# Performance work log

Measured on AMD Instinct MI355X. Metric: run time of the kernel, lower is better.

Reference implementation:

```python
import jax, jax.numpy as jnp
import numpy as np

NL, NK = 10000, 2000          # ligand / keypoint node counts
ELL, EKL = 320000, 160000     # lig->lig and kp->lig edge counts
IN, HID, OUT = 128, 128, 128  # in_size, hidden_size, out_size
FDIM = 2 * IN + 1             # edge MLP input: [h_src, h_dst, dij]


def silu(x):
    return x * jax.nn.sigmoid(x)


def setup_inputs() -> dict:
    keys = iter(jax.random.split(jax.random.key(0), 64))

    def nrm(shape, scale=0.02):
        return jax.random.normal(next(keys), shape, dtype=jnp.float32) * scale

    d = {}
    d["h_lig"] = jax.random.normal(next(keys), (NL, IN), dtype=jnp.float32)
    d["h_kp"] = jax.random.normal(next(keys), (NK, IN), dtype=jnp.float32)
    d["x_lig"] = jax.random.normal(next(keys), (NL, 3), dtype=jnp.float32)
    d["x_kp"] = jax.random.normal(next(keys), (NK, 3), dtype=jnp.float32)
    # per-node normalizer (e.g. neighbor count); keep >= 1 to avoid blowup
    d["z_lig"] = jax.random.uniform(next(keys), (NL, 1), dtype=jnp.float32, minval=1.0, maxval=32.0)
    for e in ("ll", "kl"):
        d[e + "_eW1"] = nrm((FDIM, HID)); d[e + "_eb1"] = jnp.zeros((HID,), jnp.float32)
        d[e + "_eW2"] = nrm((HID, HID)); d[e + "_eb2"] = jnp.zeros((HID,), jnp.float32)
        d[e + "_aW"] = nrm((HID, 1)); d[e + "_ab"] = jnp.zeros((1,), jnp.float32)
        d[e + "_cW1"] = nrm((FDIM, HID)); d[e + "_cb1"] = jnp.zeros((HID,), jnp.float32)
        d[e + "_cW2"] = nrm((HID, HID)); d[e + "_cb2"] = jnp.zeros((HID,), jnp.float32)
        d[e + "_cW3"] = nrm((HID, 1), scale=0.001)  # xavier gain=0.001 final coord layer
    d["n_W1"] = nrm((IN + HID, HID)); d["n_b1"] = jnp.zeros((HID,), jnp.float32)
    d["n_W2"] = nrm((HID, OUT)); d["n_b2"] = jnp.zeros((OUT,), jnp.float32)
    d["ll_src"] = jax.random.randint(next(keys), (ELL,), 0, NL, dtype=jnp.int32)
    d["ll_dst"] = jax.random.randint(next(keys), (ELL,), 0, NL, dtype=jnp.int32)
    d["kl_src"] = jax.random.randint(next(keys), (EKL,), 0, NK, dtype=jnp.int32)
    d["kl_dst"] = jax.random.randint(next(keys), (EKL,), 0, NL, dtype=jnp.int32)
    return d


def _edge_messages(hs, hd, xs, xd, eW1, eb1, eW2, eb2, aW, ab, cW1, cb1, cW2, cb2, cW3):
    x_diff = xs - xd                                     # fn.u_sub_v
    dij = jnp.linalg.norm(x_diff, axis=1, keepdims=True)  # [E,1]
    x_diff = x_diff / (dij + 1.0)
    f = jnp.concatenate([hs, hd, dij], axis=1)           # [E, 2*IN+1]
    m = silu(f @ eW1 + eb1)
    m = silu(m @ eW2 + eb2)
    msg_h = m * jax.nn.sigmoid(m @ aW + ab)              # soft attention gate
    c = silu(f @ cW1 + cb1)
    c = silu(c @ cW2 + cb2)
    msg_x = (c @ cW3) * x_diff                           # use_tanh=False path
    return msg_h, msg_x


def reference(h_lig, h_kp, x_lig, x_kp, z_lig,
              ll_eW1, ll_eb1, ll_eW2, ll_eb2, ll_aW, ll_ab,
              ll_cW1, ll_cb1, ll_cW2, ll_cb2, ll_cW3,
              kl_eW1, kl_eb1, kl_eW2, kl_eb2, kl_aW, kl_ab,
              kl_cW1, kl_cb1, kl_cW2, kl_cb2, kl_cW3,
              n_W1, n_b1, n_W2, n_b2,
              ll_src, ll_dst, kl_src, kl_dst):
    # lig -> lig edges
    mh_ll, mx_ll = _edge_messages(h_lig[ll_src], h_lig[ll_dst], x_lig[ll_src], x_lig[ll_dst],
                                  ll_eW1, ll_eb1, ll_eW2, ll_eb2, ll_aW, ll_ab,
                                  ll_cW1, ll_cb1, ll_cW2, ll_cb2, ll_cW3)
    # kp -> lig edges
    mh_kl, mx_kl = _edge_messages(h_kp[kl_src], h_lig[kl_dst], x_kp[kl_src], x_lig[kl_dst],
                                  kl_eW1, kl_eb1, kl_eW2, kl_eb2, kl_aW, kl_ab,
                                  kl_cW1, kl_cb1, kl_cW2, kl_cb2, kl_cW3)
    nl = h_lig.shape[0]
    # multi_update_all with cross_reducer='sum', then per-node normalization by z
    h_neigh = (jax.ops.segment_sum(mh_ll, ll_dst, num_segments=nl)
               + jax.ops.segment_sum(mh_kl, kl_dst, num_segments=nl)) / z_lig
    x_neigh = (jax.ops.segment_sum(mx_ll, ll_dst, num_segments=nl)
               + jax.ops.segment_sum(mx_kl, kl_dst, num_segments=nl)) / z_lig
    nin = jnp.concatenate([h_lig, h_neigh], axis=1)
    h_out = h_lig + (silu(nin @ n_W1 + n_b1) @ n_W2 + n_b2)  # norm=False -> Identity
    x_out = x_lig + x_neigh
    return (h_out, x_out)
```

## Files before the change

kernel.cpp:

```cpp
#include <hip/hip_runtime.h>
#include <hip/hip_bf16.h>
#include <math.h>

#define EPB  32
#define MSTR 136
#define FSTR 264

typedef __attribute__((ext_vector_type(8))) short short8;
typedef __attribute__((ext_vector_type(4))) float f32x4;

__device__ __forceinline__ unsigned short f2bf(float x) {
    unsigned int u = __float_as_uint(x);
    u += 0x7fffu + ((u >> 16) & 1u);
    return (unsigned short)(u >> 16);
}
__device__ __forceinline__ float bf2f(short v) {
    return __uint_as_float(((unsigned int)(unsigned short)v) << 16);
}
__device__ __forceinline__ unsigned int pkbf(float a, float b) {
    __hip_bfloat162 h = __float22bfloat162_rn(make_float2(a, b));
    union { __hip_bfloat162 h2; unsigned int u; } cv; cv.h2 = h; return cv.u;
}
__device__ __forceinline__ float frcp(float x) { return __builtin_amdgcn_rcpf(x); }
__device__ __forceinline__ float fsilu(float x) {
    return x * frcp(1.0f + __expf(-x));
}
__device__ __forceinline__ float fsigm(float x) {
    return frcp(1.0f + __expf(-x));
}
__device__ __forceinline__ void atomAddF(float* p, float v) {
    unsafeAtomicAdd(p, v);
}

struct PrepArgs { const float* src[10]; };

__global__ __launch_bounds__(256) void prep_hist_kernel(PrepArgs pa, short* __restrict__ wsb,
                                                        const int* __restrict__ lld,
                                                        const int* __restrict__ kld,
                                                        int* __restrict__ hist) {
    int idx = blockIdx.x * 256 + threadIdx.x;
    if (idx < 245760) {
        int pair = idx / 49152;
        int rem  = idx - pair * 49152;
        int second = (rem >= 32768) ? 1 : 0;
        int mi = pair * 2 + second;
        int within = second ? (rem - 32768) : rem;
        int n, k, K;
        if (second) { K = 128; n = within >> 7; k = within & 127; }
        else        { K = 256; n = within >> 8; k = within & 255; }
        int dstoff = pair * 49152 + second * 32768;
        wsb[dstoff + n * K + k] = (short)f2bf(pa.src[mi][k * 128 + n]);
        return;
    }
    idx -= 245760;
    if (idx < 320000) { atomicAdd(&hist[lld[idx]], 1); return; }
    idx -= 320000;
    if (idx < 160000) atomicAdd(&hist[10000 + kld[idx]], 1);
}

__global__ __launch_bounds__(256) void scan_kernel(const int* __restrict__ hist,
                                                   int* __restrict__ cursor) {
    __shared__ int bins[10000];
    __shared__ int ps[256];
    const int b = blockIdx.x, t = threadIdx.x;
    const int* h = hist + b * 10000;
    int* cur = cursor + b * 10000;
    for (int i = t; i < 10000; i += 256) bins[i] = h[i];
    __syncthreads();
    const int base = t * 40;
    int s = 0;
#pragma unroll 8
    for (int i = 0; i < 40; i++) { int ii = base + i; if (ii < 10000) s += bins[ii]; }
    ps[t] = s;
    __syncthreads();
    for (int off = 1; off < 256; off <<= 1) {
        int v = (t >= off) ? ps[t - off] : 0;
        __syncthreads();
        ps[t] += v;
        __syncthreads();
    }
    int run = ps[t] - s;
    for (int i = 0; i < 40; i++) {
        int ii = base + i;
        if (ii < 10000) { int c = bins[ii]; bins[ii] = run; run += c; }
    }
    __syncthreads();
    for (int i = t; i < 10000; i += 256) cur[i] = bins[i];
}

struct ProjDesc { const float* A; const short* Bt; short* out; const float* bias;
                  int rows; int ktb; int co; int hasb; };
struct CArgs {
    const int *lls, *lld, *kls, *kld;
    int* cursor;
    int *ll_ssrc, *ll_sdst, *kl_ssrc, *kl_sdst;
    ProjDesc d[8];
};

__global__ __launch_bounds__(256) void scatter_proj_kernel(CArgs ca) {
    __shared__ __align__(16) short a_lds[64 * MSTR];
    const int t = threadIdx.x;
    if (blockIdx.x < 1875) {
        int i = blockIdx.x * 256 + t;
        if (i < 320000) {
            int d = ca.lld[i];
            int p = atomicAdd(&ca.cursor[d], 1);
            ca.ll_ssrc[p] = ca.lls[i]; ca.ll_sdst[p] = d;
        } else if (i < 480000) {
            int j = i - 320000;
            int d = ca.kld[j];
            int p = atomicAdd(&ca.cursor[10000 + d], 1);
            ca.kl_ssrc[p] = ca.kls[j]; ca.kl_sdst[p] = d;
        }
        return;
    }
    const int pb = blockIdx.x - 1875;
    const int di = pb / 157, tile = pb - di * 157;
    const ProjDesc pd = ca.d[di];
    if (tile * 64 >= pd.rows) return;
    {
        const int r = t >> 2, q = t & 3;
        const int node = tile * 64 + r;
        short* arow = a_lds + r * MSTR + q * 32;
        if (node < pd.rows) {
            const float* ap = pd.A + (size_t)node * 128 + q * 32;
#pragma unroll
            for (int i = 0; i < 4; i++) {
                float4 v0 = *(const float4*)(ap + i * 8);
                float4 v1 = *(const float4*)(ap + i * 8 + 4);
                uint4 o;
                o.x = pkbf(v0.x, v0.y); o.y = pkbf(v0.z, v0.w);
                o.z = pkbf(v1.x, v1.y); o.w = pkbf(v1.z, v1.w);
                *(uint4*)(arow + i * 8) = o;
            }
        } else {
            uint4 z = make_uint4(0, 0, 0, 0);
#pragma unroll
            for (int i = 0; i < 4; i++) *(uint4*)(arow + i * 8) = z;
        }
    }
    __syncthreads();

    const int ln = t & 63, wv = t >> 6;
    const int lrow = ln & 15, quad = ln >> 4;
    const int c0 = wv * 32 + lrow, c1 = c0 + 16;

    short8 bf0[4], bf1[4];
#pragma unroll
    for (int kt = 0; kt < 4; kt++) {
        bf0[kt] = *(const short8*)(pd.Bt + c0 * 256 + (pd.ktb + kt) * 32 + quad * 8);
        bf1[kt] = *(const short8*)(pd.Bt + c1 * 256 + (pd.ktb + kt) * 32 + quad * 8);
    }
    const float bb0 = pd.hasb ? pd.bias[c0] : 0.0f;
    const float bb1 = pd.hasb ? pd.bias[c1] : 0.0f;
#pragma unroll
    for (int mt = 0; mt < 4; mt++) {
        short8 af[4];
#pragma unroll
        for (int kt = 0; kt < 4; kt++)
            af[kt] = *(const short8*)(&a_lds[(mt * 16 + lrow) * MSTR + kt * 32 + quad * 8]);
        f32x4 a0 = {0.f, 0.f, 0.f, 0.f}, a1 = {0.f, 0.f, 0.f, 0.f};
#pragma unroll
        for (int kt = 0; kt < 4; kt++) {
            a0 = __builtin_amdgcn_mfma_f32_16x16x32_bf16(af[kt], bf0[kt], a0, 0, 0, 0);
            a1 = __builtin_amdgcn_mfma_f32_16x16x32_bf16(af[kt], bf1[kt], a1, 0, 0, 0);
        }
#pragma unroll
        for (int r = 0; r < 4; r++) {
            const int node = tile * 64 + mt * 16 + quad * 4 + r;
            if (node < pd.rows) {
                pd.out[(size_t)node * 256 + pd.co + c0] = (short)f2bf(a0[r] + bb0);
                pd.out[(size_t)node * 256 + pd.co + c1] = (short)f2bf(a1[r] + bb1);
            }
        }
    }
}

struct EdgeSet {
    const short *Ps, *Pd;
    const float *xs, *xd;
    const int *esrc, *edst;
    const float *w256e, *w256c;
    const short *W2t, *cW2t;
    const float *b2e, *b2c;
    const float *aW, *ab, *cW3;
};
struct EdgePair { EdgeSet s[2]; int split; };

__global__ __launch_bounds__(256, 8) void edge_kernel(EdgePair ep,
                                                      float* __restrict__ hne,
                                                      float* __restrict__ xne)
{
    __shared__ __align__(16) char mbuf[EPB * MSTR * 4];
    __shared__ float sv_l[EPB];
    __shared__ float gate_l[EPB];
    __shared__ float xdf[3][EPB];
    __shared__ int   dstl[EPB];
    __shared__ float gpc[4][EPB];
    __shared__ float gpe[4][EPB];

    short* mh = (short*)mbuf;
    short* mc = (short*)(mbuf + EPB * MSTR * 2);
    float* msg = (float*)mbuf;

    const int isKL = (blockIdx.x >= ep.split) ? 1 : 0;
    const EdgeSet P = ep.s[isKL];
    const int eb = (blockIdx.x - (isKL ? ep.split : 0)) * EPB;
    const int t = threadIdx.x;

    {
        const int e = t >> 3, q = t & 7;
        const int eid = eb + e;
        const int s = P.esrc[eid], d = P.edst[eid];
        float dx = P.xs[s * 3 + 0] - P.xd[d * 3 + 0];
        float dy = P.xs[s * 3 + 1] - P.xd[d * 3 + 1];
        float dz = P.xs[s * 3 + 2] - P.xd[d * 3 + 2];
        float dd = __builtin_amdgcn_sqrtf(dx * dx + dy * dy + dz * dz);
        if (q == 0) {
            dstl[e] = d;
            float inv = frcp(dd + 1.0f);
            xdf[0][e] = dx * inv; xdf[1][e] = dy * inv; xdf[2][e] = dz * inv;
        }
        const short* psrow = P.Ps + (size_t)s * 256 + q * 16;
        const short* pdrow = P.Pd + (size_t)d * 256 + q * 16;
#pragma unroll
        for (int path = 0; path < 2; path++) {
            const short* ps = psrow + path * 128;
            const short* pq = pdrow + path * 128;
            const float* wq = (path ? P.w256c : P.w256e) + q * 16;
            short* mrow = (path ? mc : mh) + e * MSTR + q * 16;
#pragma unroll
            for (int i = 0; i < 2; i++) {
                short8 a = *(const short8*)(ps + i * 8);
                short8 b = *(const short8*)(pq + i * 8);
                float4 wA = *(const float4*)(wq + i * 8);
                float4 wB = *(const float4*)(wq + i * 8 + 4);
                float v0 = fsilu(bf2f(a[0]) + bf2f(b[0]) + dd * wA.x);
                float v1 = fsilu(bf2f(a[1]) + bf2f(b[1]) + dd * wA.y);
                float v2 = fsilu(bf2f(a[2]) + bf2f(b[2]) + dd * wA.z);
                float v3 = fsilu(bf2f(a[3]) + bf2f(b[3]) + dd * wA.w);
                float v4 = fsilu(bf2f(a[4]) + bf2f(b[4]) + dd * wB.x);
                float v5 = fsilu(bf2f(a[5]) + bf2f(b[5]) + dd * wB.y);
                float v6 = fsilu(bf2f(a[6]) + bf2f(b[6]) + dd * wB.z);
                float v7 = fsilu(bf2f(a[7]) + bf2f(b[7]) + dd * wB.w);
                uint4 o;
                o.x = pkbf(v0, v1); o.y = pkbf(v2, v3);
                o.z = pkbf(v4, v5); o.w = pkbf(v6, v7);
                *(uint4*)(mrow + i * 8) = o;
            }
        }
    }
    __syncthreads();

    const int ln = t & 63, wv = t >> 6;
    const int lrow = ln & 15, quad = ln >> 4;
    const int c0 = wv * 32 + lrow, c1 = c0 + 16;

    {
        short8 bf0[4], bf1[4];
#pragma unroll
        for (int kt = 0; kt < 4; kt++) {
            bf0[kt] = *(const short8*)(P.cW2t + c0 * 128 + kt * 32 + quad * 8);
            bf1[kt] = *(const short8*)(P.cW2t + c1 * 128 + kt * 32 + quad * 8);
        }
        const float cw0 = P.cW3[c0], cw1 = P.cW3[c1];
        const float bb0 = P.b2c[c0], bb1 = P.b2c[c1];
#pragma unroll
        for (int mt = 0; mt < 2; mt++) {
            short8 af[4];
#pragma unroll
            for (int kt = 0; kt < 4; kt++)
                af[kt] = *(const short8*)(&mc[(mt * 16 + lrow) * MSTR + kt * 32 + quad * 8]);
            f32x4 a0 = {0.f, 0.f, 0.f, 0.f}, a1 = {0.f, 0.f, 0.f, 0.f};
#pragma unroll
            for (int kt = 0; kt < 4; kt++) {
                a0 = __builtin_amdgcn_mfma_f32_16x16x32_bf16(af[kt], bf0[kt], a0, 0, 0, 0);
                a1 = __builtin_amdgcn_mfma_f32_16x16x32_bf16(af[kt], bf1[kt], a1, 0, 0, 0);
            }
#pragma unroll
            for (int r = 0; r < 4; r++) {
                float v0 = fsilu(a0[r] + bb0);
                float v1 = fsilu(a1[r] + bb1);
                float g = v0 * cw0 + v1 * cw1;
                g += __shfl_xor(g, 1, 64);
                g += __shfl_xor(g, 2, 64);
                g += __shfl_xor(g, 4, 64);
                g += __shfl_xor(g, 8, 64);
                if (lrow == 0) gpc[wv][mt * 16 + quad * 4 + r] = g;
            }
        }
    }

    float m2s[2][8];
    {
        short8 bf0[4], bf1[4];
#pragma unroll
        for (int kt = 0; kt < 4; kt++) {
            bf0[kt] = *(const short8*)(P.W2t + c0 * 128 + kt * 32 + quad * 8);
            bf1[kt] = *(const short8*)(P.W2t + c1 * 128 + kt * 32 + quad * 8);
        }
        const float aw0 = P.aW[c0], aw1 = P.aW[c1];
        const float bb0 = P.b2e[c0], bb1 = P.b2e[c1];
#pragma unroll
        for (int mt = 0; mt < 2; mt++) {
            short8 af[4];
#pragma unroll
            for (int kt = 0; kt < 4; kt++)
                af[kt] = *(const short8*)(&mh[(mt * 16 + lrow) * MSTR + kt * 32 + quad * 8]);
            f32x4 a0 = {0.f, 0.f, 0.f, 0.f}, a1 = {0.f, 0.f, 0.f, 0.f};
#pragma unroll
            for (int kt = 0; kt < 4; kt++) {
                a0 = __builtin_amdgcn_mfma_f32_16x16x32_bf16(af[kt], bf0[kt], a0, 0, 0, 0);
                a1 = __builtin_amdgcn_mfma_f32_16x16x32_bf16(af[kt], bf1[kt], a1, 0, 0, 0);
            }
#pragma unroll
            for (int r = 0; r < 4; r++) {
                float v0 = fsilu(a0[r] + bb0);
                float v1 = fsilu(a1[r] + bb1);
                m2s[mt][r] = v0; m2s[mt][4 + r] = v1;
                float g = v0 * aw0 + v1 * aw1;
                g += __shfl_xor(g, 1, 64);
                g += __shfl_xor(g, 2, 64);
                g += __shfl_xor(g, 4, 64);
                g += __shfl_xor(g, 8, 64);
                if (lrow == 0) gpe[wv][mt * 16 + quad * 4 + r] = g;
            }
        }
    }
    __syncthreads();

    if (t < EPB) {
        sv_l[t]   = gpc[0][t] + gpc[1][t] + gpc[2][t] + gpc[3][t];
        gate_l[t] = fsigm(gpe[0][t] + gpe[1][t] + gpe[2][t] + gpe[3][t] + P.ab[0]);
    }
#pragma unroll
    for (int mt = 0; mt < 2; mt++)
#pragma unroll
        for (int r = 0; r < 4; r++) {
            const int erow = mt * 16 + quad * 4 + r;
            msg[erow * 132 + c0] = m2s[mt][r];
            msg[erow * 132 + c1] = m2s[mt][4 + r];
        }
    __syncthreads();

    if (t < 128) {
        const int col = t;
        float acc = 0.0f;
        int cur = dstl[0];
#pragma unroll 4
        for (int e = 0; e < EPB; e++) {
            const int d = dstl[e];
            if (d != cur) {
                atomAddF(&hne[(size_t)cur * 128 + col], acc);
                acc = 0.0f; cur = d;
            }
            acc += msg[e * 132 + col] * gate_l[e];
        }
        atomAddF(&hne[(size_t)cur * 128 + col], acc);
    } else if (t < 131) {
        const int ax = t - 128;
        float acc = 0.0f;
        int cur = dstl[0];
        for (int e = 0; e < EPB; e++) {
            const int d = dstl[e];
            if (d != cur) {
                atomAddF(&xne[cur * 3 + ax], acc);
                acc = 0.0f; cur = d;
            }
            acc += sv_l[e] * xdf[ax][e];
        }
        atomAddF(&xne[cur * 3 + ax], acc);
    }
}

__global__ __launch_bounds__(256) void node_kernel(
    const float* __restrict__ h_lig, const float* __restrict__ zlig,
    const short* __restrict__ W1t, const float* __restrict__ b1v,
    const short* __restrict__ W2t, const float* __restrict__ b2v,
    const float* __restrict__ x_lig,
    const float* __restrict__ acc_h, const float* __restrict__ acc_x,
    float* __restrict__ h_out, float* __restrict__ x_out)
{
    __shared__ __align__(16) short f_lds[64 * FSTR];
    __shared__ __align__(16) short m_lds[64 * MSTR];
    const int t = threadIdx.x;
    const int nb = blockIdx.x * 64;

    {
        const int e = t >> 2, q = t & 3;
        const int node = nb + e;
        short* frow = &f_lds[e * FSTR + q * 32];
        if (node < 10000) {
            const float zi = frcp(zlig[node]);
            const float4* hp = (const float4*)(h_lig + (size_t)node * 128 + q * 32);
            const float4* np = (const float4*)(acc_h + (size_t)node * 128 + q * 32);
#pragma unroll
            for (int i = 0; i < 8; i++) {
                float4 v = hp[i];
                *(uint2*)(frow + i * 4) = make_uint2(pkbf(v.x, v.y), pkbf(v.z, v.w));
            }
#pragma unroll
            for (int i = 0; i < 8; i++) {
                float4 v = np[i];
                *(uint2*)(frow + 128 + i * 4) =
                    make_uint2(pkbf(v.x * zi, v.y * zi), pkbf(v.z * zi, v.w * zi));
            }
        } else {
            const uint2 zz = make_uint2(0, 0);
#pragma unroll
            for (int i = 0; i < 8; i++) {
                *(uint2*)(frow + i * 4) = zz;
                *(uint2*)(frow + 128 + i * 4) = zz;
            }
        }
    }
    __syncthreads();

    const int ln = t & 63, wv = t >> 6;
    const int lrow = ln & 15, quad = ln >> 4;
    const int c0 = wv * 32 + lrow, c1 = c0 + 16;

    {
        short8 bf0[8], bf1[8];
#pragma unroll
        for (int kt = 0; kt < 8; kt++) {
            bf0[kt] = *(const short8*)(W1t + c0 * 256 + kt * 32 + quad * 8);
            bf1[kt] = *(const short8*)(W1t + c1 * 256 + kt * 32 + quad * 8);
        }
        const float bb0 = b1v[c0], bb1 = b1v[c1];
#pragma unroll
        for (int mt = 0; mt < 4; mt++) {
            short8 af[8];
#pragma unroll
            for (int kt = 0; kt < 8; kt++)
                af[kt] = *(const short8*)(&f_lds[(mt * 16 + lrow) * FSTR + kt * 32 + quad * 8]);
            f32x4 a0 = {0.f, 0.f, 0.f, 0.f}, a1 = {0.f, 0.f, 0.f, 0.f};
#pragma unroll
            for (int kt = 0; kt < 8; kt++) {
                a0 = __builtin_amdgcn_mfma_f32_16x16x32_bf16(af[kt], bf0[kt], a0, 0, 0, 0);
                a1 = __builtin_amdgcn_mfma_f32_16x16x32_bf16(af[kt], bf1[kt], a1, 0, 0, 0);
            }
#pragma unroll
            for (int r = 0; r < 4; r++) {
                const int erow = mt * 16 + quad * 4 + r;
                m_lds[erow * MSTR + c0] = (short)f2bf(fsilu(a0[r] + bb0));
                m_lds[erow * MSTR + c1] = (short)f2bf(fsilu(a1[r] + bb1));
            }
        }
    }
    __syncthreads();

    {
        short8 bf0[4], bf1[4];
#pragma unroll
        for (int kt = 0; kt < 4; kt++) {
            bf0[kt] = *(const short8*)(W2t + c0 * 128 + kt * 32 + quad * 8);
            bf1[kt] = *(const short8*)(W2t + c1 * 128 + kt * 32 + quad * 8);
        }
        const float bb0 = b2v[c0], bb1 = b2v[c1];
#pragma unroll
        for (int mt = 0; mt < 4; mt++) {
            short8 af[4];
#pragma unroll
            for (int kt = 0; kt < 4; kt++)
                af[kt] = *(const short8*)(&m_lds[(mt * 16 + lrow) * MSTR + kt * 32 + quad * 8]);
            f32x4 a0 = {0.f, 0.f, 0.f, 0.f}, a1 = {0.f, 0.f, 0.f, 0.f};
#pragma unroll
            for (int kt = 0; kt < 4; kt++) {
                a0 = __builtin_amdgcn_mfma_f32_16x16x32_bf16(af[kt], bf0[kt], a0, 0, 0, 0);
                a1 = __builtin_amdgcn_mfma_f32_16x16x32_bf16(af[kt], bf1[kt], a1, 0, 0, 0);
            }
#pragma unroll
            for (int r = 0; r < 4; r++) {
                const int node = nb + mt * 16 + quad * 4 + r;
                if (node < 10000) {
                    h_out[(size_t)node * 128 + c0] = a0[r] + bb0 + h_lig[(size_t)node * 128 + c0];
                    h_out[(size_t)node * 128 + c1] = a1[r] + bb1 + h_lig[(size_t)node * 128 + c1];
                }
            }
        }
    }
    if (t < 64) {
        const int node = nb + t;
        if (node < 10000) {
            const float zi = frcp(zlig[node]);
#pragma unroll
            for (int i = 0; i < 3; i++)
                x_out[node * 3 + i] = x_lig[node * 3 + i] + acc_x[node * 3 + i] * zi;
        }
    }
}

extern "C" void kernel_launch(void* const* d_in, const int* in_sizes, int n_in,
                              void* d_out, int out_size, void* d_ws, size_t ws_size,
                              hipStream_t stream)
{
    (void)in_sizes; (void)n_in; (void)ws_size; (void)out_size;
    const float* h_lig  = (const float*)d_in[0];
    const float* h_kp   = (const float*)d_in[1];
    const float* x_lig  = (const float*)d_in[2];
    const float* x_kp   = (const float*)d_in[3];
    const float* z_lig  = (const float*)d_in[4];
    const float* ll_eW1 = (const float*)d_in[5];
    const float* ll_eb1 = (const float*)d_in[6];
    const float* ll_eW2 = (const float*)d_in[7];
    const float* ll_eb2 = (const float*)d_in[8];
    const float* ll_aW  = (const float*)d_in[9];
    const float* ll_ab  = (const float*)d_in[10];
    const float* ll_cW1 = (const float*)d_in[11];
    const float* ll_cb1 = (const float*)d_in[12];
    const float* ll_cW2 = (const float*)d_in[13];
    const float* ll_cb2 = (const float*)d_in[14];
    const float* ll_cW3 = (const float*)d_in[15];
    const float* kl_eW1 = (const float*)d_in[16];
    const float* kl_eb1 = (const float*)d_in[17];
    const float* kl_eW2 = (const float*)d_in[18];
    const float* kl_eb2 = (const float*)d_in[19];
    const float* kl_aW  = (const float*)d_in[20];
    const float* kl_ab  = (const float*)d_in[21];
    const float* kl_cW1 = (const float*)d_in[22];
    const float* kl_cb1 = (const float*)d_in[23];
    const float* kl_cW2 = (const float*)d_in[24];
    const float* kl_cb2 = (const float*)d_in[25];
    const float* kl_cW3 = (const float*)d_in[26];
    const float* n_W1   = (const float*)d_in[27];
    const float* n_b1   = (const float*)d_in[28];
    const float* n_W2   = (const float*)d_in[29];
    const float* n_b2   = (const float*)d_in[30];
    const int* ll_src = (const int*)d_in[31];
    const int* ll_dst = (const int*)d_in[32];
    const int* kl_src = (const int*)d_in[33];
    const int* kl_dst = (const int*)d_in[34];

    float* h_out = (float*)d_out;
    float* x_out = h_out + 1280000;

    char* wsc = (char*)d_ws;
    short* wsb    = (short*)wsc;
    short* P_ll_s = (short*)(wsc +   491520);
    short* P_ll_d = (short*)(wsc +  5611520);
    short* P_kl_s = (short*)(wsc + 10731520);
    short* P_kl_d = (short*)(wsc + 11755520);
    int* ll_ssrc  = (int*)(wsc + 16875520);
    int* ll_sdst  = (int*)(wsc + 18155520);
    int* kl_ssrc  = (int*)(wsc + 19435520);
    int* kl_sdst  = (int*)(wsc + 20075520);
    int* hist     = (int*)(wsc + 20715520);
    int* cursor   = (int*)(wsc + 20795520);
    float* hne    = (float*)(wsc + 20875520);
    float* xne    = (float*)(wsc + 25995520);

    hipMemsetAsync(hne, 0, 5240000, stream);
    hipMemsetAsync(hist, 0, 80000, stream);

    {
        PrepArgs pa;
        pa.src[0] = ll_eW1; pa.src[1] = ll_eW2; pa.src[2] = ll_cW1; pa.src[3] = ll_cW2;
        pa.src[4] = kl_eW1; pa.src[5] = kl_eW2; pa.src[6] = kl_cW1; pa.src[7] = kl_cW2;
        pa.src[8] = n_W1;   pa.src[9] = n_W2;
        prep_hist_kernel<<<2835, 256, 0, stream>>>(pa, wsb, ll_dst, kl_dst, hist);
    }
    scan_kernel<<<2, 256, 0, stream>>>(hist, cursor);
    {
        CArgs ca;
        ca.lls = ll_src; ca.lld = ll_dst; ca.kls = kl_src; ca.kld = kl_dst;
        ca.cursor = cursor;
        ca.ll_ssrc = ll_ssrc; ca.ll_sdst = ll_sdst;
        ca.kl_ssrc = kl_ssrc; ca.kl_sdst = kl_sdst;
        ca.d[0] = { h_lig, wsb + 0,      P_ll_s, ll_eb1, 10000, 0, 0,   0 };
        ca.d[1] = { h_lig, wsb + 49152,  P_ll_s, ll_cb1, 10000, 0, 128, 0 };
        ca.d[2] = { h_lig, wsb + 0,      P_ll_d, ll_eb1, 10000, 4, 0,   1 };
        ca.d[3] = { h_lig, wsb + 49152,  P_ll_d, ll_cb1, 10000, 4, 128, 1 };
        ca.d[4] = { h_kp,  wsb + 98304,  P_kl_s, kl_eb1,  2000, 0, 0,   0 };
        ca.d[5] = { h_kp,  wsb + 147456, P_kl_s, kl_cb1,  2000, 0, 128, 0 };
        ca.d[6] = { h_lig, wsb + 98304,  P_kl_d, kl_eb1, 10000, 4, 0,   1 };
        ca.d[7] = { h_lig, wsb + 147456, P_kl_d, kl_cb1, 10000, 4, 128, 1 };
        scatter_proj_kernel<<<1875 + 8 * 157, 256, 0, stream>>>(ca);
    }
    {
        EdgePair ep;
        ep.split = 10000;
        ep.s[0] = { P_ll_s, P_ll_d, x_lig, x_lig, ll_ssrc, ll_sdst,
                    ll_eW1 + 256 * 128, ll_cW1 + 256 * 128,
                    wsb + 32768, wsb + 81920, ll_eb2, ll_cb2,
                    ll_aW, ll_ab, ll_cW3 };
        ep.s[1] = { P_kl_s, P_kl_d, x_kp, x_lig, kl_ssrc, kl_sdst,
                    kl_eW1 + 256 * 128, kl_cW1 + 256 * 128,
                    wsb + 131072, wsb + 180224, kl_eb2, kl_cb2,
                    kl_aW, kl_ab, kl_cW3 };
        edge_kernel<<<15000, 256, 0, stream>>>(ep, hne, xne);
    }
    node_kernel<<<157, 256, 0, stream>>>(
        h_lig, z_lig, wsb + 196608, n_b1, wsb + 229376, n_b2,
        x_lig, hne, xne, h_out, x_out);
}
```

Baseline: 401.0 us.

## Fuse prep, scan, scatter, projection and edge stages into one cooperative persistent kernel

Replaces the memsets and the four separate launches (prep/hist, scan, scatter+projection, edge) with one cooperative persistent kernel that separates the phases with grid-wide syncs. The persistent blocks loop over the former block ranges of each stage, and the original multi-kernel path remains as a fallback if the cooperative launch is unavailable. The aim is to remove launch gaps and tail effects between stages. In exchange it caps occupancy at 4 blocks per CU, adds grid.sync costs, and runs the scan on only 2 blocks while the rest of the grid works on projection. It also queries device attributes and occupancy on the host every call.

```diff
diff --git a/kernel.cpp b/kernel.cpp
--- a/kernel.cpp
+++ b/kernel.cpp
@@ -1,6 +1,9 @@
 #include <hip/hip_runtime.h>
 #include <hip/hip_bf16.h>
+#include <hip/hip_cooperative_groups.h>
 #include <math.h>
+
+namespace cg = cooperative_groups;
 
 #define EPB  32
 #define MSTR 136
@@ -31,6 +34,19 @@
 __device__ __forceinline__ void atomAddF(float* p, float v) {
     unsafeAtomicAdd(p, v);
 }
+
+struct ProjDesc { const float* A; const short* Bt; short* out; const float* bias;
+                  int rows; int ktb; int co; int hasb; };
+
+struct EdgeSet {
+    const short *Ps, *Pd;
+    const float *xs, *xd;
+    const int *esrc, *edst;
+    const float *w256e, *w256c;
+    const short *W2t, *cW2t;
+    const float *b2e, *b2c;
+    const float *aW, *ab, *cW3;
+};
 
 struct PrepArgs { const float* src[10]; };
 
@@ -88,8 +104,6 @@
     for (int i = t; i < 10000; i += 256) cur[i] = bins[i];
 }
 
-struct ProjDesc { const float* A; const short* Bt; short* out; const float* bias;
-                  int rows; int ktb; int co; int hasb; };
 struct CArgs {
     const int *lls, *lld, *kls, *kld;
     int* cursor;
@@ -176,15 +190,6 @@
     }
 }
 
-struct EdgeSet {
-    const short *Ps, *Pd;
-    const float *xs, *xd;
-    const int *esrc, *edst;
-    const float *w256e, *w256c;
-    const short *W2t, *cW2t;
-    const float *b2e, *b2c;
-    const float *aW, *ab, *cW3;
-};
 struct EdgePair { EdgeSet s[2]; int split; };
 
 __global__ __launch_bounds__(256, 8) void edge_kernel(EdgePair ep,
@@ -370,6 +375,333 @@
             acc += sv_l[e] * xdf[ax][e];
         }
         atomAddF(&xne[cur * 3 + ax], acc);
+    }
+}
+
+struct MegaArgs {
+    const float* wsrc[10];
+    short* wsb;
+    const int *lls, *lld, *kls, *kld;
+    int *hist, *cursor;
+    int *ll_ssrc, *ll_sdst, *kl_ssrc, *kl_sdst;
+    float *hne, *xne;
+    ProjDesc d[8];
+    EdgeSet es[2];
+};
+
+__global__ __launch_bounds__(256, 4) void mega_kernel(MegaArgs A) {
+    __shared__ __align__(16) char smem[19968];
+    const int t = threadIdx.x;
+    const int bid = blockIdx.x;
+    const int G = gridDim.x;
+    cg::grid_group grid = cg::this_grid();
+
+    for (int i = bid * 256 + t; i < 1310000; i += G * 256) A.hne[i] = 0.0f;
+    for (int i = bid * 256 + t; i < 20000; i += G * 256) A.hist[i] = 0;
+    grid.sync();
+
+    for (int idx = bid * 256 + t; idx < 725760; idx += G * 256) {
+        if (idx < 245760) {
+            int pair = idx / 49152;
+            int rem  = idx - pair * 49152;
+            int second = (rem >= 32768) ? 1 : 0;
+            int mi = pair * 2 + second;
+            int within = second ? (rem - 32768) : rem;
+            int n, k, K;
+            if (second) { K = 128; n = within >> 7; k = within & 127; }
+            else        { K = 256; n = within >> 8; k = within & 255; }
+            int dstoff = pair * 49152 + second * 32768;
+            A.wsb[dstoff + n * K + k] = (short)f2bf(A.wsrc[mi][k * 128 + n]);
+        } else {
+            int j = idx - 245760;
+            if (j < 320000) atomicAdd(&A.hist[A.lld[j]], 1);
+            else            atomicAdd(&A.hist[10000 + A.kld[j - 320000]], 1);
+        }
+    }
+    grid.sync();
+
+    if (bid < 2) {
+        int* ps = (int*)smem;
+        const int* h = A.hist + bid * 10000;
+        int* cur = A.cursor + bid * 10000;
+        const int base = t * 40;
+        int s = 0;
+#pragma unroll 8
+        for (int i = 0; i < 40; i++) { int ii = base + i; if (ii < 10000) s += h[ii]; }
+        ps[t] = s;
+        __syncthreads();
+        for (int off = 1; off < 256; off <<= 1) {
+            int v = (t >= off) ? ps[t - off] : 0;
+            __syncthreads();
+            ps[t] += v;
+            __syncthreads();
+        }
+        int run = ps[t] - s;
+        for (int i = 0; i < 40; i++) {
+            int ii = base + i;
+            if (ii < 10000) { cur[ii] = run; run += h[ii]; }
+        }
+    } else {
+        short* a_lds = (short*)smem;
+        for (int pb = bid - 2; pb < 1256; pb += G - 2) {
+            const int di = pb / 157, tile = pb - di * 157;
+            const ProjDesc pd = A.d[di];
+            if (tile * 64 < pd.rows) {
+                {
+                    const int r = t >> 2, q = t & 3;
+                    const int node = tile * 64 + r;
+                    short* arow = a_lds + r * MSTR + q * 32;
+                    if (node < pd.rows) {
+                        const float* ap = pd.A + (size_t)node * 128 + q * 32;
+#pragma unroll
+                        for (int i = 0; i < 4; i++) {
+                            float4 v0 = *(const float4*)(ap + i * 8);
+                            float4 v1 = *(const float4*)(ap + i * 8 + 4);
+                            uint4 o;
+                            o.x = pkbf(v0.x, v0.y); o.y = pkbf(v0.z, v0.w);
+                            o.z = pkbf(v1.x, v1.y); o.w = pkbf(v1.z, v1.w);
+                            *(uint4*)(arow + i * 8) = o;
+                        }
+                    } else {
+                        uint4 z = make_uint4(0, 0, 0, 0);
+#pragma unroll
+                        for (int i = 0; i < 4; i++) *(uint4*)(arow + i * 8) = z;
+                    }
+                }
+                __syncthreads();
+                const int ln = t & 63, wv = t >> 6;
+                const int lrow = ln & 15, quad = ln >> 4;
+                const int c0 = wv * 32 + lrow, c1 = c0 + 16;
+                short8 bf0[4], bf1[4];
+#pragma unroll
+                for (int kt = 0; kt < 4; kt++) {
+                    bf0[kt] = *(const short8*)(pd.Bt + c0 * 256 + (pd.ktb + kt) * 32 + quad * 8);
+                    bf1[kt] = *(const short8*)(pd.Bt + c1 * 256 + (pd.ktb + kt) * 32 + quad * 8);
+                }
+                const float bb0 = pd.hasb ? pd.bias[c0] : 0.0f;
+                const float bb1 = pd.hasb ? pd.bias[c1] : 0.0f;
+#pragma unroll
+                for (int mt = 0; mt < 4; mt++) {
+                    short8 af[4];
+#pragma unroll
+                    for (int kt = 0; kt < 4; kt++)
+                        af[kt] = *(const short8*)(&a_lds[(mt * 16 + lrow) * MSTR + kt * 32 + quad * 8]);
+                    f32x4 a0 = {0.f, 0.f, 0.f, 0.f}, a1 = {0.f, 0.f, 0.f, 0.f};
+#pragma unroll
+                    for (int kt = 0; kt < 4; kt++) {
+                        a0 = __builtin_amdgcn_mfma_f32_16x16x32_bf16(af[kt], bf0[kt], a0, 0, 0, 0);
+                        a1 = __builtin_amdgcn_mfma_f32_16x16x32_bf16(af[kt], bf1[kt], a1, 0, 0, 0);
+                    }
+#pragma unroll
+                    for (int r = 0; r < 4; r++) {
+                        const int node = tile * 64 + mt * 16 + quad * 4 + r;
+                        if (node < pd.rows) {
+                            pd.out[(size_t)node * 256 + pd.co + c0] = (short)f2bf(a0[r] + bb0);
+                            pd.out[(size_t)node * 256 + pd.co + c1] = (short)f2bf(a1[r] + bb1);
+                        }
+                    }
+                }
+            }
+            __syncthreads();
+        }
+    }
+    grid.sync();
+
+    for (int i = bid * 256 + t; i < 480000; i += G * 256) {
+        if (i < 320000) {
+            int d = A.lld[i];
+            int p = atomicAdd(&A.cursor[d], 1);
+            A.ll_ssrc[p] = A.lls[i]; A.ll_sdst[p] = d;
+        } else {
+            int j = i - 320000;
+            int d = A.kld[j];
+            int p = atomicAdd(&A.cursor[10000 + d], 1);
+            A.kl_ssrc[p] = A.kls[j]; A.kl_sdst[p] = d;
+        }
+    }
+    grid.sync();
+
+    short* mh  = (short*)smem;
+    short* mc  = (short*)(smem + 8704);
+    float* msg = (float*)smem;
+    float* sv_l   = (float*)(smem + 17408);
+    float* gate_l = (float*)(smem + 17536);
+    float* xdf    = (float*)(smem + 17664);
+    int*   dstl   = (int*)(smem + 18048);
+    float* gpc    = (float*)(smem + 18176);
+    float* gpe    = (float*)(smem + 18688);
+
+    const int ln = t & 63, wv = t >> 6;
+    const int lrow = ln & 15, quad = ln >> 4;
+    const int c0 = wv * 32 + lrow, c1 = c0 + 16;
+
+    for (int vb = bid; vb < 15000; vb += G) {
+        const int isKL = (vb >= 10000) ? 1 : 0;
+        const EdgeSet P = A.es[isKL];
+        const int eb = (isKL ? vb - 10000 : vb) * EPB;
+
+        {
+            const int e = t >> 3, q = t & 7;
+            const int eid = eb + e;
+            const int s = P.esrc[eid], d = P.edst[eid];
+            float dx = P.xs[s * 3 + 0] - P.xd[d * 3 + 0];
+            float dy = P.xs[s * 3 + 1] - P.xd[d * 3 + 1];
+            float dz = P.xs[s * 3 + 2] - P.xd[d * 3 + 2];
+            float dd = __builtin_amdgcn_sqrtf(dx * dx + dy * dy + dz * dz);
+            if (q == 0) {
+                dstl[e] = d;
+                float inv = frcp(dd + 1.0f);
+                xdf[0 * EPB + e] = dx * inv;
+                xdf[1 * EPB + e] = dy * inv;
+                xdf[2 * EPB + e] = dz * inv;
+            }
+            const short* psrow = P.Ps + (size_t)s * 256 + q * 16;
+            const short* pdrow = P.Pd + (size_t)d * 256 + q * 16;
+#pragma unroll
+            for (int path = 0; path < 2; path++) {
+                const short* ps = psrow + path * 128;
+                const short* pq = pdrow + path * 128;
+                const float* wq = (path ? P.w256c : P.w256e) + q * 16;
+                short* mrow = (path ? mc : mh) + e * MSTR + q * 16;
+#pragma unroll
+                for (int i = 0; i < 2; i++) {
+                    short8 a = *(const short8*)(ps + i * 8);
+                    short8 b = *(const short8*)(pq + i * 8);
+                    float4 wA = *(const float4*)(wq + i * 8);
+                    float4 wB = *(const float4*)(wq + i * 8 + 4);
+                    float v0 = fsilu(bf2f(a[0]) + bf2f(b[0]) + dd * wA.x);
+                    float v1 = fsilu(bf2f(a[1]) + bf2f(b[1]) + dd * wA.y);
+                    float v2 = fsilu(bf2f(a[2]) + bf2f(b[2]) + dd * wA.z);
+                    float v3 = fsilu(bf2f(a[3]) + bf2f(b[3]) + dd * wA.w);
+                    float v4 = fsilu(bf2f(a[4]) + bf2f(b[4]) + dd * wB.x);
+                    float v5 = fsilu(bf2f(a[5]) + bf2f(b[5]) + dd * wB.y);
+                    float v6 = fsilu(bf2f(a[6]) + bf2f(b[6]) + dd * wB.z);
+                    float v7 = fsilu(bf2f(a[7]) + bf2f(b[7]) + dd * wB.w);
+                    uint4 o;
+                    o.x = pkbf(v0, v1); o.y = pkbf(v2, v3);
+                    o.z = pkbf(v4, v5); o.w = pkbf(v6, v7);
+                    *(uint4*)(mrow + i * 8) = o;
+                }
+            }
+        }
+        __syncthreads();
+
+        {
+            short8 bf0[4], bf1[4];
+#pragma unroll
+            for (int kt = 0; kt < 4; kt++) {
+                bf0[kt] = *(const short8*)(P.cW2t + c0 * 128 + kt * 32 + quad * 8);
+                bf1[kt] = *(const short8*)(P.cW2t + c1 * 128 + kt * 32 + quad * 8);
+            }
+            const float cw0 = P.cW3[c0], cw1 = P.cW3[c1];
+            const float bb0 = P.b2c[c0], bb1 = P.b2c[c1];
+#pragma unroll
+            for (int mt = 0; mt < 2; mt++) {
+                short8 af[4];
+#pragma unroll
+                for (int kt = 0; kt < 4; kt++)
+                    af[kt] = *(const short8*)(&mc[(mt * 16 + lrow) * MSTR + kt * 32 + quad * 8]);
+                f32x4 a0 = {0.f, 0.f, 0.f, 0.f}, a1 = {0.f, 0.f, 0.f, 0.f};
+#pragma unroll
+                for (int kt = 0; kt < 4; kt++) {
+                    a0 = __builtin_amdgcn_mfma_f32_16x16x32_bf16(af[kt], bf0[kt], a0, 0, 0, 0);
+                    a1 = __builtin_amdgcn_mfma_f32_16x16x32_bf16(af[kt], bf1[kt], a1, 0, 0, 0);
+                }
+#pragma unroll
+                for (int r = 0; r < 4; r++) {
+                    float v0 = fsilu(a0[r] + bb0);
+                    float v1 = fsilu(a1[r] + bb1);
+                    float g = v0 * cw0 + v1 * cw1;
+                    g += __shfl_xor(g, 1, 64);
+                    g += __shfl_xor(g, 2, 64);
+                    g += __shfl_xor(g, 4, 64);
+                    g += __shfl_xor(g, 8, 64);
+                    if (lrow == 0) gpc[wv * EPB + mt * 16 + quad * 4 + r] = g;
+                }
+            }
+        }
+
+        float m2s[2][8];
+        {
+            short8 bf0[4], bf1[4];
+#pragma unroll
+            for (int kt = 0; kt < 4; kt++) {
+                bf0[kt] = *(const short8*)(P.W2t + c0 * 128 + kt * 32 + quad * 8);
+                bf1[kt] = *(const short8*)(P.W2t + c1 * 128 + kt * 32 + quad * 8);
+            }
+            const float aw0 = P.aW[c0], aw1 = P.aW[c1];
+            const float bb0 = P.b2e[c0], bb1 = P.b2e[c1];
+#pragma unroll
+            for (int mt = 0; mt < 2; mt++) {
+                short8 af[4];
+#pragma unroll
+                for (int kt = 0; kt < 4; kt++)
+                    af[kt] = *(const short8*)(&mh[(mt * 16 + lrow) * MSTR + kt * 32 + quad * 8]);
+                f32x4 a0 = {0.f, 0.f, 0.f, 0.f}, a1 = {0.f, 0.f, 0.f, 0.f};
+#pragma unroll
+                for (int kt = 0; kt < 4; kt++) {
+                    a0 = __builtin_amdgcn_mfma_f32_16x16x32_bf16(af[kt], bf0[kt], a0, 0, 0, 0);
+                    a1 = __builtin_amdgcn_mfma_f32_16x16x32_bf16(af[kt], bf1[kt], a1, 0, 0, 0);
+                }
+#pragma unroll
+                for (int r = 0; r < 4; r++) {
+                    float v0 = fsilu(a0[r] + bb0);
+                    float v1 = fsilu(a1[r] + bb1);
+                    m2s[mt][r] = v0; m2s[mt][4 + r] = v1;
+                    float g = v0 * aw0 + v1 * aw1;
+                    g += __shfl_xor(g, 1, 64);
+                    g += __shfl_xor(g, 2, 64);
+                    g += __shfl_xor(g, 4, 64);
+                    g += __shfl_xor(g, 8, 64);
+                    if (lrow == 0) gpe[wv * EPB + mt * 16 + quad * 4 + r] = g;
+                }
+            }
+        }
+        __syncthreads();
+
+        if (t < EPB) {
+            sv_l[t]   = gpc[0 * EPB + t] + gpc[1 * EPB + t] + gpc[2 * EPB + t] + gpc[3 * EPB + t];
+            gate_l[t] = fsigm(gpe[0 * EPB + t] + gpe[1 * EPB + t] + gpe[2 * EPB + t] + gpe[3 * EPB + t] + P.ab[0]);
+        }
+#pragma unroll
+        for (int mt = 0; mt < 2; mt++)
+#pragma unroll
+            for (int r = 0; r < 4; r++) {
+                const int erow = mt * 16 + quad * 4 + r;
+                msg[erow * 132 + c0] = m2s[mt][r];
+                msg[erow * 132 + c1] = m2s[mt][4 + r];
+            }
+        __syncthreads();
+
+        if (t < 128) {
+            const int col = t;
+            float acc = 0.0f;
+            int cur = dstl[0];
+#pragma unroll 4
+            for (int e = 0; e < EPB; e++) {
+                const int d = dstl[e];
+                if (d != cur) {
+                    atomAddF(&A.hne[(size_t)cur * 128 + col], acc);
+                    acc = 0.0f; cur = d;
+                }
+                acc += msg[e * 132 + col] * gate_l[e];
+            }
+            atomAddF(&A.hne[(size_t)cur * 128 + col], acc);
+        } else if (t < 131) {
+            const int ax = t - 128;
+            float acc = 0.0f;
+            int cur = dstl[0];
+            for (int e = 0; e < EPB; e++) {
+                const int d = dstl[e];
+                if (d != cur) {
+                    atomAddF(&A.xne[cur * 3 + ax], acc);
+                    acc = 0.0f; cur = d;
+                }
+                acc += sv_l[e] * xdf[ax * EPB + e];
+            }
+            atomAddF(&A.xne[cur * 3 + ax], acc);
+        }
+        __syncthreads();
     }
 }
 
@@ -550,46 +882,78 @@
     float* hne    = (float*)(wsc + 20875520);
     float* xne    = (float*)(wsc + 25995520);
 
-    hipMemsetAsync(hne, 0, 5240000, stream);
-    hipMemsetAsync(hist, 0, 80000, stream);
-
-    {
+    ProjDesc pdv[8];
+    pdv[0] = { h_lig, wsb + 0,      P_ll_s, ll_eb1, 10000, 0, 0,   0 };
+    pdv[1] = { h_lig, wsb + 49152,  P_ll_s, ll_cb1, 10000, 0, 128, 0 };
+    pdv[2] = { h_lig, wsb + 0,      P_ll_d, ll_eb1, 10000, 4, 0,   1 };
+    pdv[3] = { h_lig, wsb + 49152,  P_ll_d, ll_cb1, 10000, 4, 128, 1 };
+    pdv[4] = { h_kp,  wsb + 98304,  P_kl_s, kl_eb1,  2000, 0, 0,   0 };
+    pdv[5] = { h_kp,  wsb + 147456, P_kl_s, kl_cb1,  2000, 0, 128, 0 };
+    pdv[6] = { h_lig, wsb + 98304,  P_kl_d, kl_eb1, 10000, 4, 0,   1 };
+    pdv[7] = { h_lig, wsb + 147456, P_kl_d, kl_cb1, 10000, 4, 128, 1 };
+
+    EdgeSet es0 = { P_ll_s, P_ll_d, x_lig, x_lig, ll_ssrc, ll_sdst,
+                    ll_eW1 + 256 * 128, ll_cW1 + 256 * 128,
+                    wsb + 32768, wsb + 81920, ll_eb2, ll_cb2,
+                    ll_aW, ll_ab, ll_cW3 };
+    EdgeSet es1 = { P_kl_s, P_kl_d, x_kp, x_lig, kl_ssrc, kl_sdst,
+                    kl_eW1 + 256 * 128, kl_cW1 + 256 * 128,
+                    wsb + 131072, wsb + 180224, kl_eb2, kl_cb2,
+                    kl_aW, kl_ab, kl_cW3 };
+
+    bool coop_ok = true;
+    int cus = 0, perCU = 0;
+    if (hipDeviceGetAttribute(&cus, hipDeviceAttributeMultiprocessorCount, 0) != hipSuccess
+        || cus <= 0) coop_ok = false;
+    if (coop_ok &&
+        hipOccupancyMaxActiveBlocksPerMultiprocessor(&perCU, (const void*)mega_kernel,
+                                                     256, 0) != hipSuccess) coop_ok = false;
+    int grid = coop_ok ? perCU * cus : 0;
+    if (grid < 3) coop_ok = false;
+
+    if (coop_ok) {
+        MegaArgs ma;
+        for (int i = 0; i < 8; i++) ma.d[i] = pdv[i];
+        ma.wsrc[0] = ll_eW1; ma.wsrc[1] = ll_eW2; ma.wsrc[2] = ll_cW1; ma.wsrc[3] = ll_cW2;
+        ma.wsrc[4] = kl_eW1; ma.wsrc[5] = kl_eW2; ma.wsrc[6] = kl_cW1; ma.wsrc[7] = kl_cW2;
+        ma.wsrc[8] = n_W1;   ma.wsrc[9] = n_W2;
+        ma.wsb = wsb;
+        ma.lls = ll_src; ma.lld = ll_dst; ma.kls = kl_src; ma.kld = kl_dst;
+        ma.hist = hist; ma.cursor = cursor;
+        ma.ll_ssrc = ll_ssrc; ma.ll_sdst = ll_sdst;
+        ma.kl_ssrc = kl_ssrc; ma.kl_sdst = kl_sdst;
+        ma.hne = hne; ma.xne = xne;
+        ma.es[0] = es0; ma.es[1] = es1;
+        void* kargs[] = { (void*)&ma };
+        if (hipLaunchCooperativeKernel((void*)mega_kernel, dim3(grid), dim3(256),
+                                       kargs, 0, stream) != hipSuccess) {
+            coop_ok = false;
+            (void)hipGetLastError();
+        }
+    }
+
+    if (!coop_ok) {
+        hipMemsetAsync(hne, 0, 5240000, stream);
+        hipMemsetAsync(hist, 0, 80000, stream);
         PrepArgs pa;
         pa.src[0] = ll_eW1; pa.src[1] = ll_eW2; pa.src[2] = ll_cW1; pa.src[3] = ll_cW2;
         pa.src[4] = kl_eW1; pa.src[5] = kl_eW2; pa.src[6] = kl_cW1; pa.src[7] = kl_cW2;
         pa.src[8] = n_W1;   pa.src[9] = n_W2;
         prep_hist_kernel<<<2835, 256, 0, stream>>>(pa, wsb, ll_dst, kl_dst, hist);
-    }
-    scan_kernel<<<2, 256, 0, stream>>>(hist, cursor);
-    {
+        scan_kernel<<<2, 256, 0, stream>>>(hist, cursor);
         CArgs ca;
         ca.lls = ll_src; ca.lld = ll_dst; ca.kls = kl_src; ca.kld = kl_dst;
         ca.cursor = cursor;
         ca.ll_ssrc = ll_ssrc; ca.ll_sdst = ll_sdst;
         ca.kl_ssrc = kl_ssrc; ca.kl_sdst = kl_sdst;
-        ca.d[0] = { h_lig, wsb + 0,      P_ll_s, ll_eb1, 10000, 0, 0,   0 };
-        ca.d[1] = { h_lig, wsb + 49152,  P_ll_s, ll_cb1, 10000, 0, 128, 0 };
-        ca.d[2] = { h_lig, wsb + 0,      P_ll_d, ll_eb1, 10000, 4, 0,   1 };
-        ca.d[3] = { h_lig, wsb + 49152,  P_ll_d, ll_cb1, 10000, 4, 128, 1 };
-        ca.d[4] = { h_kp,  wsb + 98304,  P_kl_s, kl_eb1,  2000, 0, 0,   0 };
-        ca.d[5] = { h_kp,  wsb + 147456, P_kl_s, kl_cb1,  2000, 0, 128, 0 };
-        ca.d[6] = { h_lig, wsb + 98304,  P_kl_d, kl_eb1, 10000, 4, 0,   1 };
-        ca.d[7] = { h_lig, wsb + 147456, P_kl_d, kl_cb1, 10000, 4, 128, 1 };
+        for (int i = 0; i < 8; i++) ca.d[i] = pdv[i];
         scatter_proj_kernel<<<1875 + 8 * 157, 256, 0, stream>>>(ca);
-    }
-    {
         EdgePair ep;
         ep.split = 10000;
-        ep.s[0] = { P_ll_s, P_ll_d, x_lig, x_lig, ll_ssrc, ll_sdst,
-                    ll_eW1 + 256 * 128, ll_cW1 + 256 * 128,
-                    wsb + 32768, wsb + 81920, ll_eb2, ll_cb2,
-                    ll_aW, ll_ab, ll_cW3 };
-        ep.s[1] = { P_kl_s, P_kl_d, x_kp, x_lig, kl_ssrc, kl_sdst,
-                    kl_eW1 + 256 * 128, kl_cW1 + 256 * 128,
-                    wsb + 131072, wsb + 180224, kl_eb2, kl_cb2,
-                    kl_aW, kl_ab, kl_cW3 };
+        ep.s[0] = es0; ep.s[1] = es1;
         edge_kernel<<<15000, 256, 0, stream>>>(ep, hne, xne);
     }
+
     node_kernel<<<157, 256, 0, stream>>>(
         h_lig, z_lig, wsb + 196608, n_b1, wsb + 229376, n_b2,
         x_lig, hne, xne, h_out, x_out);
```

New measurement: 813.9 us. 103% more time.

## Fold hne memset into prep kernel and overlap projections with scan and scatter

Applied to the files above, without the earlier changes.

Zeroing of the hne/xne accumulators moves from a separate memset into a grid-stride loop at the start of the prep/histogram kernel. The 8x157 projection GEMM tiles are split in half: the first 628 tiles run in a new kernel alongside the two-block prefix scan (which now reads hist directly from global memory instead of staging in LDS), and the remaining 628 run alongside the edge scatter. This removes one launch and a memset, and lets the mostly idle scan step share the GPU with useful GEMM work. In exchange, the scan's repeated global reads may be slower than the LDS version.

```diff
diff --git a/kernel.cpp b/kernel.cpp
--- a/kernel.cpp
+++ b/kernel.cpp
@@ -32,12 +32,81 @@
     unsafeAtomicAdd(p, v);
 }
 
+struct ProjDesc { const float* A; const short* Bt; short* out; const float* bias;
+                  int rows; int ktb; int co; int hasb; };
+
+__device__ __forceinline__ void proj_body(const ProjDesc* dv, int pb, int t, short* a_lds) {
+    const int di = pb / 157, tile = pb - di * 157;
+    const ProjDesc pd = dv[di];
+    if (tile * 64 >= pd.rows) return;
+    {
+        const int r = t >> 2, q = t & 3;
+        const int node = tile * 64 + r;
+        short* arow = a_lds + r * MSTR + q * 32;
+        if (node < pd.rows) {
+            const float* ap = pd.A + (size_t)node * 128 + q * 32;
+#pragma unroll
+            for (int i = 0; i < 4; i++) {
+                float4 v0 = *(const float4*)(ap + i * 8);
+                float4 v1 = *(const float4*)(ap + i * 8 + 4);
+                uint4 o;
+                o.x = pkbf(v0.x, v0.y); o.y = pkbf(v0.z, v0.w);
+                o.z = pkbf(v1.x, v1.y); o.w = pkbf(v1.z, v1.w);
+                *(uint4*)(arow + i * 8) = o;
+            }
+        } else {
+            uint4 z = make_uint4(0, 0, 0, 0);
+#pragma unroll
+            for (int i = 0; i < 4; i++) *(uint4*)(arow + i * 8) = z;
+        }
+    }
+    __syncthreads();
+
+    const int ln = t & 63, wv = t >> 6;
+    const int lrow = ln & 15, quad = ln >> 4;
+    const int c0 = wv * 32 + lrow, c1 = c0 + 16;
+
+    short8 bf0[4], bf1[4];
+#pragma unroll
+    for (int kt = 0; kt < 4; kt++) {
+        bf0[kt] = *(const short8*)(pd.Bt + c0 * 256 + (pd.ktb + kt) * 32 + quad * 8);
+        bf1[kt] = *(const short8*)(pd.Bt + c1 * 256 + (pd.ktb + kt) * 32 + quad * 8);
+    }
+    const float bb0 = pd.hasb ? pd.bias[c0] : 0.0f;
+    const float bb1 = pd.hasb ? pd.bias[c1] : 0.0f;
+#pragma unroll
+    for (int mt = 0; mt < 4; mt++) {
+        short8 af[4];
+#pragma unroll
+        for (int kt = 0; kt < 4; kt++)
+            af[kt] = *(const short8*)(&a_lds[(mt * 16 + lrow) * MSTR + kt * 32 + quad * 8]);
+        f32x4 a0 = {0.f, 0.f, 0.f, 0.f}, a1 = {0.f, 0.f, 0.f, 0.f};
+#pragma unroll
+        for (int kt = 0; kt < 4; kt++) {
+            a0 = __builtin_amdgcn_mfma_f32_16x16x32_bf16(af[kt], bf0[kt], a0, 0, 0, 0);
+            a1 = __builtin_amdgcn_mfma_f32_16x16x32_bf16(af[kt], bf1[kt], a1, 0, 0, 0);
+        }
+#pragma unroll
+        for (int r = 0; r < 4; r++) {
+            const int node = tile * 64 + mt * 16 + quad * 4 + r;
+            if (node < pd.rows) {
+                pd.out[(size_t)node * 256 + pd.co + c0] = (short)f2bf(a0[r] + bb0);
+                pd.out[(size_t)node * 256 + pd.co + c1] = (short)f2bf(a1[r] + bb1);
+            }
+        }
+    }
+}
+
 struct PrepArgs { const float* src[10]; };
 
 __global__ __launch_bounds__(256) void prep_hist_kernel(PrepArgs pa, short* __restrict__ wsb,
                                                         const int* __restrict__ lld,
                                                         const int* __restrict__ kld,
-                                                        int* __restrict__ hist) {
+                                                        int* __restrict__ hist,
+                                                        float* __restrict__ hne) {
+    const int G = gridDim.x * 256;
+    for (int i = blockIdx.x * 256 + threadIdx.x; i < 1310000; i += G) hne[i] = 0.0f;
+
     int idx = blockIdx.x * 256 + threadIdx.x;
     if (idx < 245760) {
         int pair = idx / 49152;
@@ -58,38 +127,38 @@
     if (idx < 160000) atomicAdd(&hist[10000 + kld[idx]], 1);
 }
 
-__global__ __launch_bounds__(256) void scan_kernel(const int* __restrict__ hist,
-                                                   int* __restrict__ cursor) {
-    __shared__ int bins[10000];
-    __shared__ int ps[256];
-    const int b = blockIdx.x, t = threadIdx.x;
-    const int* h = hist + b * 10000;
-    int* cur = cursor + b * 10000;
-    for (int i = t; i < 10000; i += 256) bins[i] = h[i];
-    __syncthreads();
-    const int base = t * 40;
-    int s = 0;
+struct SPArgs { const int* hist; int* cursor; ProjDesc d[8]; };
+
+__global__ __launch_bounds__(256) void scan_proj_kernel(SPArgs sp) {
+    __shared__ __align__(16) short a_lds[64 * MSTR];
+    const int t = threadIdx.x;
+    if (blockIdx.x < 2) {
+        int* ps = (int*)a_lds;
+        const int b = blockIdx.x;
+        const int* h = sp.hist + b * 10000;
+        int* cur = sp.cursor + b * 10000;
+        const int base = t * 40;
+        int s = 0;
 #pragma unroll 8
-    for (int i = 0; i < 40; i++) { int ii = base + i; if (ii < 10000) s += bins[ii]; }
-    ps[t] = s;
-    __syncthreads();
-    for (int off = 1; off < 256; off <<= 1) {
-        int v = (t >= off) ? ps[t - off] : 0;
+        for (int i = 0; i < 40; i++) { int ii = base + i; if (ii < 10000) s += h[ii]; }
+        ps[t] = s;
         __syncthreads();
-        ps[t] += v;
-        __syncthreads();
-    }
-    int run = ps[t] - s;
-    for (int i = 0; i < 40; i++) {
-        int ii = base + i;
-        if (ii < 10000) { int c = bins[ii]; bins[ii] = run; run += c; }
-    }
-    __syncthreads();
-    for (int i = t; i < 10000; i += 256) cur[i] = bins[i];
-}
-
-struct ProjDesc { const float* A; const short* Bt; short* out; const float* bias;
-                  int rows; int ktb; int co; int hasb; };
+        for (int off = 1; off < 256; off <<= 1) {
+            int v = (t >= off) ? ps[t - off] : 0;
+            __syncthreads();
+            ps[t] += v;
+            __syncthreads();
+        }
+        int run = ps[t] - s;
+        for (int i = 0; i < 40; i++) {
+            int ii = base + i;
+            if (ii < 10000) { cur[ii] = run; run += h[ii]; }
+        }
+        return;
+    }
+    proj_body(sp.d, blockIdx.x - 2, t, a_lds);
+}
+
 struct CArgs {
     const int *lls, *lld, *kls, *kld;
     int* cursor;
@@ -114,66 +183,7 @@
         }
         return;
     }
-    const int pb = blockIdx.x - 1875;
-    const int di = pb / 157, tile = pb - di * 157;
-    const ProjDesc pd = ca.d[di];
-    if (tile * 64 >= pd.rows) return;
-    {
-        const int r = t >> 2, q = t & 3;
-        const int node = tile * 64 + r;
-        short* arow = a_lds + r * MSTR + q * 32;
-        if (node < pd.rows) {
-            const float* ap = pd.A + (size_t)node * 128 + q * 32;
-#pragma unroll
-            for (int i = 0; i < 4; i++) {
-                float4 v0 = *(const float4*)(ap + i * 8);
-                float4 v1 = *(const float4*)(ap + i * 8 + 4);
-                uint4 o;
-                o.x = pkbf(v0.x, v0.y); o.y = pkbf(v0.z, v0.w);
-                o.z = pkbf(v1.x, v1.y); o.w = pkbf(v1.z, v1.w);
-                *(uint4*)(arow + i * 8) = o;
-            }
-        } else {
-            uint4 z = make_uint4(0, 0, 0, 0);
-#pragma unroll
-            for (int i = 0; i < 4; i++) *(uint4*)(arow + i * 8) = z;
-        }
-    }
-    __syncthreads();
-
-    const int ln = t & 63, wv = t >> 6;
-    const int lrow = ln & 15, quad = ln >> 4;
-    const int c0 = wv * 32 + lrow, c1 = c0 + 16;
-
-    short8 bf0[4], bf1[4];
-#pragma unroll
-    for (int kt = 0; kt < 4; kt++) {
-        bf0[kt] = *(const short8*)(pd.Bt + c0 * 256 + (pd.ktb + kt) * 32 + quad * 8);
-        bf1[kt] = *(const short8*)(pd.Bt + c1 * 256 + (pd.ktb + kt) * 32 + quad * 8);
-    }
-    const float bb0 = pd.hasb ? pd.bias[c0] : 0.0f;
-    const float bb1 = pd.hasb ? pd.bias[c1] : 0.0f;
-#pragma unroll
-    for (int mt = 0; mt < 4; mt++) {
-        short8 af[4];
-#pragma unroll
-        for (int kt = 0; kt < 4; kt++)
-            af[kt] = *(const short8*)(&a_lds[(mt * 16 + lrow) * MSTR + kt * 32 + quad * 8]);
-        f32x4 a0 = {0.f, 0.f, 0.f, 0.f}, a1 = {0.f, 0.f, 0.f, 0.f};
-#pragma unroll
-        for (int kt = 0; kt < 4; kt++) {
-            a0 = __builtin_amdgcn_mfma_f32_16x16x32_bf16(af[kt], bf0[kt], a0, 0, 0, 0);
-            a1 = __builtin_amdgcn_mfma_f32_16x16x32_bf16(af[kt], bf1[kt], a1, 0, 0, 0);
-        }
-#pragma unroll
-        for (int r = 0; r < 4; r++) {
-            const int node = tile * 64 + mt * 16 + quad * 4 + r;
-            if (node < pd.rows) {
-                pd.out[(size_t)node * 256 + pd.co + c0] = (short)f2bf(a0[r] + bb0);
-                pd.out[(size_t)node * 256 + pd.co + c1] = (short)f2bf(a1[r] + bb1);
-            }
-        }
-    }
+    proj_body(ca.d, 628 + (blockIdx.x - 1875), t, a_lds);
 }
 
 struct EdgeSet {
@@ -550,7 +560,16 @@
     float* hne    = (float*)(wsc + 20875520);
     float* xne    = (float*)(wsc + 25995520);
 
-    hipMemsetAsync(hne, 0, 5240000, stream);
+    ProjDesc pdv[8];
+    pdv[0] = { h_lig, wsb + 0,      P_ll_s, ll_eb1, 10000, 0, 0,   0 };
+    pdv[1] = { h_lig, wsb + 49152,  P_ll_s, ll_cb1, 10000, 0, 128, 0 };
+    pdv[2] = { h_lig, wsb + 0,      P_ll_d, ll_eb1, 10000, 4, 0,   1 };
+    pdv[3] = { h_lig, wsb + 49152,  P_ll_d, ll_cb1, 10000, 4, 128, 1 };
+    pdv[4] = { h_kp,  wsb + 98304,  P_kl_s, kl_eb1,  2000, 0, 0,   0 };
+    pdv[5] = { h_kp,  wsb + 147456, P_kl_s, kl_cb1,  2000, 0, 128, 0 };
+    pdv[6] = { h_lig, wsb + 98304,  P_kl_d, kl_eb1, 10000, 4, 0,   1 };
+    pdv[7] = { h_lig, wsb + 147456, P_kl_d, kl_cb1, 10000, 4, 128, 1 };
+
     hipMemsetAsync(hist, 0, 80000, stream);
 
     {
@@ -558,24 +577,22 @@
         pa.src[0] = ll_eW1; pa.src[1] = ll_eW2; pa.src[2] = ll_cW1; pa.src[3] = ll_cW2;
         pa.src[4] = kl_eW1; pa.src[5] = kl_eW2; pa.src[6] = kl_cW1; pa.src[7] = kl_cW2;
         pa.src[8] = n_W1;   pa.src[9] = n_W2;
-        prep_hist_kernel<<<2835, 256, 0, stream>>>(pa, wsb, ll_dst, kl_dst, hist);
-    }
-    scan_kernel<<<2, 256, 0, stream>>>(hist, cursor);
+        prep_hist_kernel<<<2835, 256, 0, stream>>>(pa, wsb, ll_dst, kl_dst, hist, hne);
+    }
+    {
+        SPArgs sp;
+        sp.hist = hist; sp.cursor = cursor;
+        for (int i = 0; i < 8; i++) sp.d[i] = pdv[i];
+        scan_proj_kernel<<<2 + 628, 256, 0, stream>>>(sp);
+    }
     {
         CArgs ca;
         ca.lls = ll_src; ca.lld = ll_dst; ca.kls = kl_src; ca.kld = kl_dst;
         ca.cursor = cursor;
         ca.ll_ssrc = ll_ssrc; ca.ll_sdst = ll_sdst;
         ca.kl_ssrc = kl_ssrc; ca.kl_sdst = kl_sdst;
-        ca.d[0] = { h_lig, wsb + 0,      P_ll_s, ll_eb1, 10000, 0, 0,   0 };
-        ca.d[1] = { h_lig, wsb + 49152,  P_ll_s, ll_cb1, 10000, 0, 128, 0 };
-        ca.d[2] = { h_lig, wsb + 0,      P_ll_d, ll_eb1, 10000, 4, 0,   1 };
-        ca.d[3] = { h_lig, wsb + 49152,  P_ll_d, ll_cb1, 10000, 4, 128, 1 };
-        ca.d[4] = { h_kp,  wsb + 98304,  P_kl_s, kl_eb1,  2000, 0, 0,   0 };
-        ca.d[5] = { h_kp,  wsb + 147456, P_kl_s, kl_cb1,  2000, 0, 128, 0 };
-        ca.d[6] = { h_lig, wsb + 98304,  P_kl_d, kl_eb1, 10000, 4, 0,   1 };
-        ca.d[7] = { h_lig, wsb + 147456, P_kl_d, kl_cb1, 10000, 4, 128, 1 };
-        scatter_proj_kernel<<<1875 + 8 * 157, 256, 0, stream>>>(ca);
+        for (int i = 0; i < 8; i++) ca.d[i] = pdv[i];
+        scatter_proj_kernel<<<1875 + 628, 256, 0, stream>>>(ca);
     }
     {
         EdgePair ep;
```

After: 411.0 us. 2.5% more time.
